# Optimization experiments

Hardware: AMD Instinct MI355X
Metric: run time of the kernel (lower is better)

Reference implementation:

```python
import math
import jax, jax.numpy as jnp
import numpy as np

ORD_Q, ORD_K = 1, 2
DIM_QK, N_HEADS = 64, 4
DH = DIM_QK // N_HEADS  # dim_qk_head = 16


def mask_tensor(order, n):
    """Bool tensor of shape [n]*order, True where all `order` indices are pairwise distinct."""
    idx = jnp.arange(n)
    m = jnp.ones((n,) * order, dtype=bool)
    for i in range(order):
        for j in range(i + 1, order):
            si = [1] * order; si[i] = n
            sj = [1] * order; sj[j] = n
            m = m & (idx.reshape(si) != idx.reshape(sj))
    return m


def setup_inputs() -> dict:
    key = jax.random.key(0)
    k1, k2, k3 = jax.random.split(key, 3)
    B, n = 4, 128
    q_A = jax.random.normal(k1, (B, n, DIM_QK), dtype=jnp.float32)
    k_A = jax.random.normal(k2, (B, n, n, DIM_QK), dtype=jnp.float32)
    node_mask = jax.random.uniform(k3, (B, n)) > 0.2   # valid-node mask
    q_mask = node_mask                                  # order-1 mask [B, n]
    k_mask = node_mask[:, :, None] & node_mask[:, None, :]  # order-2 mask [B, n, n]
    return {"q_A": q_A, "k_A": k_A, "q_mask": q_mask, "k_mask": k_mask}


def reference(q_A, k_A, q_mask, k_mask):
    B, n, D = q_A.shape
    Lq, Lk = n ** ORD_Q, n ** ORD_K
    # split heads: chunk h takes channels [h*DH:(h+1)*DH] -> [H, B, L, DH]
    q = q_A.reshape(B, Lq, N_HEADS, DH).transpose(2, 0, 1, 3)
    k = k_A.reshape(B, Lk, N_HEADS, DH).transpose(2, 0, 1, 3)
    # combinatorial all-distinct mask over ord_q+ord_k = 3 indices -> [Lq, Lk]
    M = mask_tensor(ORD_Q + ORD_K, n).reshape(Lq, Lk)
    qk_mask = q_mask.reshape(B, Lq)[:, :, None] & k_mask.reshape(B, Lk)[:, None, :]
    att_mask = (M[None] & qk_mask)[None]  # [1, B, Lq, Lk]
    sdp = jnp.einsum('hbkd,hbld->hbkl', q, k) / math.sqrt(DH)
    sdp = jnp.where(att_mask, sdp, -jnp.inf)
    alpha = jax.nn.softmax(sdp, axis=-1)
    alpha = jnp.where(att_mask, alpha, 0.0)  # also zeroes NaN rows (fully masked)
    return alpha
```

## Files before the change

### kernel.cpp

```cpp
#include <hip/hip_runtime.h>
#include <math.h>

#define BB 4
#define NN 128
#define LK 16384
#define DD 64
#define HH 4
#define DHH 16
#define TI2 32
#define KROWS 64
#define KPAD 68
#define L1CH 256
#define NL1 (LK/L1CH)
#define QK_SCALE 0.3606737602f

__device__ __forceinline__ float fexp2(float x){
#if __has_builtin(__builtin_amdgcn_exp2f)
  return __builtin_amdgcn_exp2f(x);
#else
  return __expf(x * 0.6931471806f);
#endif
}

__device__ __forceinline__ int compute_mode(const void* __restrict__ qmask){
  const unsigned int* w = (const unsigned int*)qmask;
  const int t = threadIdx.x & 63;
  int u8 = 0, i32 = 0, f32 = 0;
  #pragma unroll
  for (int rep = 0; rep < 2; ++rep){
    const unsigned int x = w[t + rep*64];
    const bool one  = (x == 1u);
    const bool fone = (x == 0x3f800000u);
    const bool nz   = (x != 0u);
    u8  += __popcll(__ballot(nz && !one && !fone));
    i32 += __popcll(__ballot(one));
    f32 += __popcll(__ballot(fone));
  }
  int mode = 0;
  if (u8 > i32 && u8 > f32) mode = 1;
  else if (f32 > i32) mode = 2;
  return mode;
}

__device__ __forceinline__ bool mget(const void* __restrict__ p, int idx, int mode){
  if (mode == 1) return ((const unsigned char*)p)[idx] != 0;
  if (mode == 2) return ((const float*)p)[idx] != 0.0f;
  return ((const int*)p)[idx] != 0;
}

__device__ __forceinline__ float dot16(float4 q0, float4 q1, float4 q2, float4 q3,
                                       float4 k0, float4 k1, float4 k2, float4 k3){
  float d;
  d = q0.x*k0.x;         d = fmaf(q0.y,k0.y,d); d = fmaf(q0.z,k0.z,d); d = fmaf(q0.w,k0.w,d);
  d = fmaf(q1.x,k1.x,d); d = fmaf(q1.y,k1.y,d); d = fmaf(q1.z,k1.z,d); d = fmaf(q1.w,k1.w,d);
  d = fmaf(q2.x,k2.x,d); d = fmaf(q2.y,k2.y,d); d = fmaf(q2.z,k2.z,d); d = fmaf(q2.w,k2.w,d);
  d = fmaf(q3.x,k3.x,d); d = fmaf(q3.y,k3.y,d); d = fmaf(q3.z,k3.z,d); d = fmaf(q3.w,k3.w,d);
  return d;
}

__device__ __forceinline__ void stage_k(const float* __restrict__ kA, int b, int lbase,
                                        float* __restrict__ ldsK){
  const int t = threadIdx.x;
  const float4* src = (const float4*)(kA + ((size_t)(b*LK + lbase))*DD);
  #pragma unroll
  for (int p = 0; p < 4; ++p){
    const int f = p*256 + t;
    const float4 v = src[f];
    *(float4*)(ldsK + (f >> 4)*KPAD + (f & 15)*4) = v;
  }
}

__device__ __forceinline__ void stage_q(const float* __restrict__ qA, int b, int ibase,
                                        float* __restrict__ ldsQ){
  const int t = threadIdx.x;
  const float4* src = (const float4*)(qA + ((size_t)(b*NN + ibase))*DD);
  #pragma unroll
  for (int p = 0; p < 2; ++p){
    const int f = p*256 + t;
    float4 v = src[f];
    v.x *= QK_SCALE; v.y *= QK_SCALE; v.z *= QK_SCALE; v.w *= QK_SCALE;
    *(float4*)(ldsQ + (f >> 4)*DD + (f & 15)*4) = v;
  }
}

__global__ __launch_bounds__(256) void k1_rowsum(
    const float* __restrict__ qA, const float* __restrict__ kA,
    const void* __restrict__ qm, const void* __restrict__ km,
    float* __restrict__ partials)
{
  __shared__ float ldsK[KROWS*KPAD];
  __shared__ float ldsQ[TI2*DD];
  __shared__ float ldsP[HH][TI2];
  const int mode = compute_mode(qm);
  const int lc = blockIdx.x, it = blockIdx.y, b = blockIdx.z;
  const int t = threadIdx.x, w = t >> 6, ll = t & 63;
  const int ibase = it*TI2;

  stage_q(qA, b, ibase, ldsQ);

  float s[TI2];
  #pragma unroll
  for (int i = 0; i < TI2; ++i) s[i] = 0.0f;

  for (int jj = 0; jj < L1CH/KROWS; ++jj){
    if (jj) __syncthreads();
    stage_k(kA, b, lc*L1CH + jj*KROWS, ldsK);
    __syncthreads();

    const int l  = lc*L1CH + jj*KROWS + ll;
    const int jn = l >> 7, kn = l & 127;
    const bool kv = (jn != kn) && mget(km, (b << 14) + l, mode);
    unsigned vmask = kv ? 0xFFFFFFFFu : 0u;
    if ((unsigned)(jn - ibase) < TI2) vmask &= ~(1u << (jn - ibase));
    if ((unsigned)(kn - ibase) < TI2) vmask &= ~(1u << (kn - ibase));

    const float* kp = ldsK + ll*KPAD + w*DHH;
    const float4 k0 = *(const float4*)(kp),    k1 = *(const float4*)(kp+4),
                 k2 = *(const float4*)(kp+8),  k3 = *(const float4*)(kp+12);

    #pragma unroll
    for (int i = 0; i < TI2; ++i){
      const float* qp = ldsQ + i*DD + w*DHH;
      float d = dot16(*(const float4*)(qp),   *(const float4*)(qp+4),
                      *(const float4*)(qp+8), *(const float4*)(qp+12),
                      k0, k1, k2, k3);
      d = (vmask & (1u << i)) ? d : -INFINITY;
      s[i] += fexp2(d);
    }
  }

  #pragma unroll
  for (int i = 0; i < TI2; ++i){
    float v = s[i];
    #pragma unroll
    for (int off = 32; off; off >>= 1) v += __shfl_xor(v, off);
    if (ll == 0) ldsP[w][i] = v;
  }
  __syncthreads();
  if (t < HH*TI2){
    const int h = t >> 5, i = t & 31;
    const bool qv = mget(qm, b*NN + ibase + i, mode);
    partials[((lc*BB + b)*HH + h)*NN + ibase + i] = qv ? ldsP[h][i] : 0.0f;
  }
}

__global__ void k1_finalize(const float* __restrict__ partials, float* __restrict__ R){
  const int tid = blockIdx.x*256 + threadIdx.x;
  float ssum = 0.0f;
  for (int lc = 0; lc < NL1; ++lc) ssum += partials[lc*(BB*HH*NN) + tid];
  R[tid] = (ssum > 0.0f) ? 1.0f/ssum : 0.0f;
}

__global__ __launch_bounds__(256) void k2_emit(
    const float* __restrict__ qA, const float* __restrict__ kA,
    const void* __restrict__ qm, const void* __restrict__ km,
    const float* __restrict__ R, float* __restrict__ out)
{
  __shared__ float ldsQ[TI2*DD];
  __shared__ float ldsR[HH*TI2];
  const int mode = compute_mode(qm);
  const int lc = blockIdx.x, it = blockIdx.y, b = blockIdx.z;
  const int t = threadIdx.x, w = t >> 6, ll = t & 63;
  const int ibase = it*TI2;
  const int lbase = lc*256 + ll*4;

  stage_q(qA, b, ibase, ldsQ);
  if (t < HH*TI2){
    ldsR[t] = R[(b*HH + (t >> 5))*NN + ibase + (t & 31)];
  }

  float4 kk[4][4];
  #pragma unroll
  for (int e = 0; e < 4; ++e){
    const float4* kp = (const float4*)(kA + ((size_t)(b*LK + lbase + e))*DD + w*DHH);
    #pragma unroll
    for (int p = 0; p < 4; ++p) kk[e][p] = kp[p];
  }

  unsigned vm[4];
  #pragma unroll
  for (int e = 0; e < 4; ++e){
    const int l = lbase + e;
    const int jn = l >> 7, kn = l & 127;
    const bool kv = (jn != kn) && mget(km, b*LK + l, mode);
    unsigned m = kv ? 0xFFFFFFFFu : 0u;
    if ((unsigned)(jn - ibase) < TI2) m &= ~(1u << (jn - ibase));
    if ((unsigned)(kn - ibase) < TI2) m &= ~(1u << (kn - ibase));
    vm[e] = m;
  }
  __syncthreads();

  float* op = out + (((size_t)((w*BB + b)*NN + ibase)) << 14) + lbase;

  #pragma unroll 2
  for (int i = 0; i < TI2; ++i){
    const float* qp = ldsQ + i*DD + w*DHH;
    const float4 q0 = *(const float4*)(qp),   q1 = *(const float4*)(qp+4),
                 q2 = *(const float4*)(qp+8), q3 = *(const float4*)(qp+12);
    const float r = ldsR[w*TI2 + i];
    float4 o;
    o.x = fexp2((vm[0] & (1u<<i)) ? dot16(q0,q1,q2,q3, kk[0][0],kk[0][1],kk[0][2],kk[0][3]) : -INFINITY) * r;
    o.y = fexp2((vm[1] & (1u<<i)) ? dot16(q0,q1,q2,q3, kk[1][0],kk[1][1],kk[1][2],kk[1][3]) : -INFINITY) * r;
    o.z = fexp2((vm[2] & (1u<<i)) ? dot16(q0,q1,q2,q3, kk[2][0],kk[2][1],kk[2][2],kk[2][3]) : -INFINITY) * r;
    o.w = fexp2((vm[3] & (1u<<i)) ? dot16(q0,q1,q2,q3, kk[3][0],kk[3][1],kk[3][2],kk[3][3]) : -INFINITY) * r;
    *(float4*)(op + (((size_t)i) << 14)) = o;
  }
}

extern "C" void kernel_launch(void* const* d_in, const int* in_sizes, int n_in,
                              void* d_out, int out_size, void* d_ws, size_t ws_size,
                              hipStream_t stream)
{
  const float* qA = (const float*)d_in[0];
  const float* kA = (const float*)d_in[1];
  const void*  qm = d_in[2];
  const void*  km = d_in[3];
  float* out = (float*)d_out;

  float* partials = (float*)d_ws;
  float* R        = partials + (size_t)NL1*BB*HH*NN;

  dim3 g1(NL1, NN/TI2, BB);
  k1_rowsum<<<g1, 256, 0, stream>>>(qA, kA, qm, km, partials);
  k1_finalize<<<(BB*HH*NN)/256, 256, 0, stream>>>(partials, R);
  dim3 g2(LK/256, NN/TI2, BB);
  k2_emit<<<g2, 256, 0, stream>>>(qA, kA, qm, km, R, out);
}
```

Measured before the change: 69.34 us.

## Merge query tiles into 1024-thread rowsum blocks sharing staged K

```diff
diff --git a/kernel.cpp b/kernel.cpp
--- a/kernel.cpp
+++ b/kernel.cpp
@@ -10,8 +10,6 @@
 #define TI2 32
 #define KROWS 64
 #define KPAD 68
-#define L1CH 256
-#define NL1 (LK/L1CH)
 #define QK_SCALE 0.3606737602f
 
 __device__ __forceinline__ float fexp2(float x){
@@ -58,18 +56,6 @@
   return d;
 }
 
-__device__ __forceinline__ void stage_k(const float* __restrict__ kA, int b, int lbase,
-                                        float* __restrict__ ldsK){
-  const int t = threadIdx.x;
-  const float4* src = (const float4*)(kA + ((size_t)(b*LK + lbase))*DD);
-  #pragma unroll
-  for (int p = 0; p < 4; ++p){
-    const int f = p*256 + t;
-    const float4 v = src[f];
-    *(float4*)(ldsK + (f >> 4)*KPAD + (f & 15)*4) = v;
-  }
-}
-
 __device__ __forceinline__ void stage_q(const float* __restrict__ qA, int b, int ibase,
                                         float* __restrict__ ldsQ){
   const int t = threadIdx.x;
@@ -83,44 +69,58 @@
   }
 }
 
-__global__ __launch_bounds__(256) void k1_rowsum(
+__global__ __launch_bounds__(1024) void k1_rowsum(
     const float* __restrict__ qA, const float* __restrict__ kA,
     const void* __restrict__ qm, const void* __restrict__ km,
     float* __restrict__ partials)
 {
   __shared__ float ldsK[KROWS*KPAD];
-  __shared__ float ldsQ[TI2*DD];
-  __shared__ float ldsP[HH][TI2];
+  __shared__ float ldsQ[NN*DD];
+  __shared__ float ldsP[16][TI2];
   const int mode = compute_mode(qm);
-  const int lc = blockIdx.x, it = blockIdx.y, b = blockIdx.z;
+  const int lc = blockIdx.x, b = blockIdx.y;
   const int t = threadIdx.x, w = t >> 6, ll = t & 63;
+  const int h = w & 3, it = w >> 2;
   const int ibase = it*TI2;
 
-  stage_q(qA, b, ibase, ldsQ);
+  {
+    const float4* src = (const float4*)(qA + ((size_t)(b*NN))*DD);
+    #pragma unroll
+    for (int p = 0; p < 2; ++p){
+      const int f = p*1024 + t;
+      float4 v = src[f];
+      v.x *= QK_SCALE; v.y *= QK_SCALE; v.z *= QK_SCALE; v.w *= QK_SCALE;
+      *(float4*)(ldsQ + (f >> 4)*DD + (f & 15)*4) = v;
+    }
+  }
 
   float s[TI2];
   #pragma unroll
   for (int i = 0; i < TI2; ++i) s[i] = 0.0f;
 
-  for (int jj = 0; jj < L1CH/KROWS; ++jj){
+  for (int jj = 0; jj < 4; ++jj){
     if (jj) __syncthreads();
-    stage_k(kA, b, lc*L1CH + jj*KROWS, ldsK);
+    {
+      const float4* src = (const float4*)(kA + ((size_t)(b*LK + lc*256 + jj*KROWS))*DD);
+      const float4 v = src[t];
+      *(float4*)(ldsK + (t >> 4)*KPAD + (t & 15)*4) = v;
+    }
     __syncthreads();
 
-    const int l  = lc*L1CH + jj*KROWS + ll;
+    const int l  = lc*256 + jj*KROWS + ll;
     const int jn = l >> 7, kn = l & 127;
     const bool kv = (jn != kn) && mget(km, (b << 14) + l, mode);
     unsigned vmask = kv ? 0xFFFFFFFFu : 0u;
     if ((unsigned)(jn - ibase) < TI2) vmask &= ~(1u << (jn - ibase));
     if ((unsigned)(kn - ibase) < TI2) vmask &= ~(1u << (kn - ibase));
 
-    const float* kp = ldsK + ll*KPAD + w*DHH;
+    const float* kp = ldsK + ll*KPAD + h*DHH;
     const float4 k0 = *(const float4*)(kp),    k1 = *(const float4*)(kp+4),
                  k2 = *(const float4*)(kp+8),  k3 = *(const float4*)(kp+12);
 
     #pragma unroll
     for (int i = 0; i < TI2; ++i){
-      const float* qp = ldsQ + i*DD + w*DHH;
+      const float* qp = ldsQ + (ibase + i)*DD + h*DHH;
       float d = dot16(*(const float4*)(qp),   *(const float4*)(qp+4),
                       *(const float4*)(qp+8), *(const float4*)(qp+12),
                       k0, k1, k2, k3);
@@ -137,17 +137,17 @@
     if (ll == 0) ldsP[w][i] = v;
   }
   __syncthreads();
-  if (t < HH*TI2){
-    const int h = t >> 5, i = t & 31;
-    const bool qv = mget(qm, b*NN + ibase + i, mode);
-    partials[((lc*BB + b)*HH + h)*NN + ibase + i] = qv ? ldsP[h][i] : 0.0f;
+  if (t < HH*NN){
+    const int h2 = t >> 7, i = t & 127;
+    const bool qv = mget(qm, b*NN + i, mode);
+    partials[((lc*BB + b)*HH + h2)*NN + i] = qv ? ldsP[(i >> 5)*4 + h2][i & 31] : 0.0f;
   }
 }
 
 __global__ void k1_finalize(const float* __restrict__ partials, float* __restrict__ R){
   const int tid = blockIdx.x*256 + threadIdx.x;
   float ssum = 0.0f;
-  for (int lc = 0; lc < NL1; ++lc) ssum += partials[lc*(BB*HH*NN) + tid];
+  for (int lc = 0; lc < LK/256; ++lc) ssum += partials[lc*(BB*HH*NN) + tid];
   R[tid] = (ssum > 0.0f) ? 1.0f/ssum : 0.0f;
 }
 
@@ -218,10 +218,10 @@
   float* out = (float*)d_out;
 
   float* partials = (float*)d_ws;
-  float* R        = partials + (size_t)NL1*BB*HH*NN;
-
-  dim3 g1(NL1, NN/TI2, BB);
-  k1_rowsum<<<g1, 256, 0, stream>>>(qA, kA, qm, km, partials);
+  float* R        = partials + (size_t)(LK/256)*BB*HH*NN;
+
+  dim3 g1(LK/256, BB);
+  k1_rowsum<<<g1, 1024, 0, stream>>>(qA, kA, qm, km, partials);
   k1_finalize<<<(BB*HH*NN)/256, 256, 0, stream>>>(partials, R);
   dim3 g2(LK/256, NN/TI2, BB);
   k2_emit<<<g2, 256, 0, stream>>>(qA, kA, qm, km, R, out);
```

New measurement: 73.53 us. 6.0% more time.

## Fuse rowsum, finalize and emit into one cooperative kernel with grid sync

Applied to the files above, without the earlier changes.

```diff
diff --git a/kernel.cpp b/kernel.cpp
--- a/kernel.cpp
+++ b/kernel.cpp
@@ -1,5 +1,8 @@
 #include <hip/hip_runtime.h>
+#include <hip/hip_cooperative_groups.h>
 #include <math.h>
+
+namespace cg = cooperative_groups;
 
 #define BB 4
 #define NN 128
@@ -10,8 +13,7 @@
 #define TI2 32
 #define KROWS 64
 #define KPAD 68
-#define L1CH 256
-#define NL1 (LK/L1CH)
+#define NL1 64
 #define QK_SCALE 0.3606737602f
 
 __device__ __forceinline__ float fexp2(float x){
@@ -80,6 +82,118 @@
     float4 v = src[f];
     v.x *= QK_SCALE; v.y *= QK_SCALE; v.z *= QK_SCALE; v.w *= QK_SCALE;
     *(float4*)(ldsQ + (f >> 4)*DD + (f & 15)*4) = v;
+  }
+}
+
+__global__ __launch_bounds__(256, 4) void fused_all(
+    const float* __restrict__ qA, const float* __restrict__ kA,
+    const void* __restrict__ qm, const void* __restrict__ km,
+    float* __restrict__ partials, float* __restrict__ out)
+{
+  __shared__ float ldsK[KROWS*KPAD];
+  __shared__ float ldsQ[TI2*DD];
+  __shared__ float ldsP[HH][TI2];
+  __shared__ float ldsR[HH*TI2];
+  const int mode = compute_mode(qm);
+  const int lc = blockIdx.x, it = blockIdx.y, b = blockIdx.z;
+  const int t = threadIdx.x, w = t >> 6, ll = t & 63;
+  const int ibase = it*TI2;
+
+  stage_q(qA, b, ibase, ldsQ);
+
+  float s[TI2];
+  #pragma unroll
+  for (int i = 0; i < TI2; ++i) s[i] = 0.0f;
+
+  for (int jj = 0; jj < 4; ++jj){
+    if (jj) __syncthreads();
+    stage_k(kA, b, lc*256 + jj*KROWS, ldsK);
+    __syncthreads();
+
+    const int l  = lc*256 + jj*KROWS + ll;
+    const int jn = l >> 7, kn = l & 127;
+    const bool kv = (jn != kn) && mget(km, (b << 14) + l, mode);
+    unsigned vmask = kv ? 0xFFFFFFFFu : 0u;
+    if ((unsigned)(jn - ibase) < TI2) vmask &= ~(1u << (jn - ibase));
+    if ((unsigned)(kn - ibase) < TI2) vmask &= ~(1u << (kn - ibase));
+
+    const float* kp = ldsK + ll*KPAD + w*DHH;
+    const float4 k0 = *(const float4*)(kp),    k1 = *(const float4*)(kp+4),
+                 k2 = *(const float4*)(kp+8),  k3 = *(const float4*)(kp+12);
+
+    #pragma unroll
+    for (int i = 0; i < TI2; ++i){
+      const float* qp = ldsQ + i*DD + w*DHH;
+      float d = dot16(*(const float4*)(qp),   *(const float4*)(qp+4),
+                      *(const float4*)(qp+8), *(const float4*)(qp+12),
+                      k0, k1, k2, k3);
+      d = (vmask & (1u << i)) ? d : -INFINITY;
+      s[i] += fexp2(d);
+    }
+  }
+
+  #pragma unroll
+  for (int i = 0; i < TI2; ++i){
+    float v = s[i];
+    #pragma unroll
+    for (int off = 32; off; off >>= 1) v += __shfl_xor(v, off);
+    if (ll == 0) ldsP[w][i] = v;
+  }
+  __syncthreads();
+  if (t < HH*TI2){
+    const int h = t >> 5, i = t & 31;
+    const bool qv = mget(qm, b*NN + ibase + i, mode);
+    partials[((lc*BB + b)*HH + h)*NN + ibase + i] = qv ? ldsP[h][i] : 0.0f;
+  }
+
+  cg::this_grid().sync();
+
+  if (t < HH*TI2){
+    const int h = t >> 5, i = t & 31;
+    const float* pp = partials + (size_t)(b*HH + h)*NN + ibase + i;
+    float ssum = 0.0f;
+    #pragma unroll 8
+    for (int lcc = 0; lcc < NL1; ++lcc) ssum += pp[(size_t)lcc*(BB*HH*NN)];
+    ldsR[t] = (ssum > 0.0f) ? 1.0f/ssum : 0.0f;
+  }
+  __syncthreads();
+
+  const int lbase = lc*256 + ll*4;
+
+  float4 kk[4][4];
+  #pragma unroll
+  for (int e = 0; e < 4; ++e){
+    const float4* kp = (const float4*)(kA + ((size_t)(b*LK + lbase + e))*DD + w*DHH);
+    #pragma unroll
+    for (int p = 0; p < 4; ++p) kk[e][p] = kp[p];
+  }
+
+  unsigned vm[4];
+  #pragma unroll
+  for (int e = 0; e < 4; ++e){
+    const int l = lbase + e;
+    const int jn = l >> 7, kn = l & 127;
+    const bool kv = (jn != kn) && mget(km, b*LK + l, mode);
+    unsigned m = kv ? 0xFFFFFFFFu : 0u;
+    if ((unsigned)(jn - ibase) < TI2) m &= ~(1u << (jn - ibase));
+    if ((unsigned)(kn - ibase) < TI2) m &= ~(1u << (kn - ibase));
+    vm[e] = m;
+  }
+
+  float* op = out + (((size_t)((w*BB + b)*NN + ibase)) << 14) + lbase;
+
+  #pragma unroll 2
+  for (int i = 0; i < TI2; ++i){
+    const float* qp = ldsQ + i*DD + w*DHH;
+    const float4 q0 = *(const float4*)(qp),   q1 = *(const float4*)(qp+4),
+                 q2 = *(const float4*)(qp+8), q3 = *(const float4*)(qp+12);
+    const float r = ldsR[w*TI2 + i];
+    float4 o;
+    o.x = fexp2((vm[0] & (1u<<i)) ? dot16(q0,q1,q2,q3, kk[0][0],kk[0][1],kk[0][2],kk[0][3]) : -INFINITY) * r;
+    o.y = fexp2((vm[1] & (1u<<i)) ? dot16(q0,q1,q2,q3, kk[1][0],kk[1][1],kk[1][2],kk[1][3]) : -INFINITY) * r;
+    o.z = fexp2((vm[2] & (1u<<i)) ? dot16(q0,q1,q2,q3, kk[2][0],kk[2][1],kk[2][2],kk[2][3]) : -INFINITY) * r;
+    o.w = fexp2((vm[3] & (1u<<i)) ? dot16(q0,q1,q2,q3, kk[3][0],kk[3][1],kk[3][2],kk[3][3]) : -INFINITY) * r;
+    *(float4*)(op + (((size_t)i) << 14)) = o;
   }
 }
 
@@ -102,12 +216,12 @@
   #pragma unroll
   for (int i = 0; i < TI2; ++i) s[i] = 0.0f;
 
-  for (int jj = 0; jj < L1CH/KROWS; ++jj){
+  for (int jj = 0; jj < 4; ++jj){
     if (jj) __syncthreads();
-    stage_k(kA, b, lc*L1CH + jj*KROWS, ldsK);
+    stage_k(kA, b, lc*256 + jj*KROWS, ldsK);
     __syncthreads();
 
-    const int l  = lc*L1CH + jj*KROWS + ll;
+    const int l  = lc*256 + jj*KROWS + ll;
     const int jn = l >> 7, kn = l & 127;
     const bool kv = (jn != kn) && mget(km, (b << 14) + l, mode);
     unsigned vmask = kv ? 0xFFFFFFFFu : 0u;
@@ -220,9 +334,16 @@
   float* partials = (float*)d_ws;
   float* R        = partials + (size_t)NL1*BB*HH*NN;
 
-  dim3 g1(NL1, NN/TI2, BB);
-  k1_rowsum<<<g1, 256, 0, stream>>>(qA, kA, qm, km, partials);
-  k1_finalize<<<(BB*HH*NN)/256, 256, 0, stream>>>(partials, R);
-  dim3 g2(LK/256, NN/TI2, BB);
-  k2_emit<<<g2, 256, 0, stream>>>(qA, kA, qm, km, R, out);
-}
+  dim3 grid(NL1, NN/TI2, BB);
+
+  void* args[6];
+  args[0] = (void*)&qA; args[1] = (void*)&kA; args[2] = (void*)&qm;
+  args[3] = (void*)&km; args[4] = (void*)&partials; args[5] = (void*)&out;
+  hipError_t err = hipLaunchCooperativeKernel((void*)fused_all, grid, dim3(256),
+                                              args, 0, stream);
+  if (err != hipSuccess){
+    k1_rowsum<<<grid, 256, 0, stream>>>(qA, kA, qm, km, partials);
+    k1_finalize<<<(BB*HH*NN)/256, 256, 0, stream>>>(partials, R);
+    k2_emit<<<grid, 256, 0, stream>>>(qA, kA, qm, km, R, out);
+  }
+}
```

Result: slower. 171.2 us (+146.9%).
